# Performance work log

Measured on AMD Instinct MI355X. Metric: run time of the kernel, lower is better.

Reference implementation:

```python
import jax, jax.numpy as jnp
import numpy as np

SIGMA = 10.0   # collision energy scale (init sigma)
LCOL = 0.5     # collision length scale (init lcol)


def setup_inputs() -> dict:
    key = jax.random.key(0)
    B, D = 64, 2050  # 64 chains, N = 1 + (D-4)/2 = 1024 beads each
    # values must be in [-0.5, 0.5]: r2 = conf + 0.5 feeds arccos(1 - 2*r2)
    confdata = jax.random.uniform(key, (B, D), dtype=jnp.float32, minval=-0.5, maxval=0.5)
    return {"confdata": confdata}


def _energy(confdata):
    # --- get_poly, batched over all chains ---
    init_pos = confdata[:, 1:4]                      # [B, 3]
    c = confdata[:, 4:] + 0.5                        # [B, 2*(N-1)] in [0, 1]
    r1, r2 = c[:, ::2], c[:, 1::2]                   # [B, N-1]
    ph = r1 * (2.0 * jnp.pi)
    th = jnp.arccos(1.0 - 2.0 * r2)
    st = jnp.sin(th)
    steps = jnp.stack([st * jnp.cos(ph), st * jnp.sin(ph), jnp.cos(th)], axis=-1)  # [B, N-1, 3]
    pos = jnp.cumsum(jnp.concatenate([init_pos[:, None, :], steps], axis=1), axis=1)  # [B, N, 3]

    # --- collisions: sum over pairs with d > 0 of exp(-(d/lcol)^2) ---
    diff = pos[:, :, None, :] - pos[:, None, :, :]   # [B, N, N, 3]; exact zeros on diagonal
    d2 = jnp.sum(diff * diff, axis=-1)               # [B, N, N]
    e = jnp.where(d2 > 0, jnp.exp(-d2 / (LCOL * LCOL)), 0.0)
    return SIGMA * jnp.sum(e)


def reference(confdata):
    return _energy(confdata)
```

## Files before the change

kernel.cpp:

```cpp
#include <hip/hip_runtime.h>

#define NPOS 1024
#define NBATCH 64
#define DROW 2050
#define NPG 18
#define NBLK (NBATCH * NPG)

__global__ __launch_bounds__(256) void fused_kernel(const float* __restrict__ conf,
                                                    float* __restrict__ part) {
  __shared__ float4 P[NPOS];
  __shared__ float wsx[4], wsy[4], wsz[4];
  __shared__ float red[4];

  const int g = blockIdx.x % NPG;
  const int b = blockIdx.x / NPG;
  const int tid = threadIdx.x;
  const int lane = tid & 63, w = tid >> 6;
  const float* __restrict__ row = conf + b * DROW;
  const float ALPHA = 2.40224481f;

  float lx[4], ly[4], lz[4];
  float rx = 0.f, ry = 0.f, rz = 0.f;
#pragma unroll
  for (int k = 0; k < 4; ++k) {
    const int n = 4 * tid + k;
    if (n > 0) {
      const float2 rr = *reinterpret_cast<const float2*>(row + 2 + 2 * n);
      const float r1 = rr.x + 0.5f;
      const float r2 = rr.y + 0.5f;
      const float ct = 1.f - 2.f * r2;
      const float st = sqrtf(fmaxf(0.f, 1.f - ct * ct));
      const float sp = __builtin_amdgcn_sinf(r1);
      const float cp = __builtin_amdgcn_cosf(r1);
      rx += st * cp; ry += st * sp; rz += ct;
    }
    lx[k] = rx; ly[k] = ry; lz[k] = rz;
  }
  const float ttx = rx, tty = ry, ttz = rz;
  float sx = rx, sy = ry, sz = rz;
#pragma unroll
  for (int off = 1; off < 64; off <<= 1) {
    const float ax = __shfl_up(sx, off, 64);
    const float ay = __shfl_up(sy, off, 64);
    const float az = __shfl_up(sz, off, 64);
    if (lane >= off) { sx += ax; sy += ay; sz += az; }
  }
  if (lane == 63) { wsx[w] = sx; wsy[w] = sy; wsz[w] = sz; }
  __syncthreads();
  float cx = 0.f, cy = 0.f, cz = 0.f;
#pragma unroll
  for (int ww = 0; ww < 3; ++ww)
    if (ww < w) { cx += wsx[ww]; cy += wsy[ww]; cz += wsz[ww]; }

  const float ox = row[1] + cx + (sx - ttx);
  const float oy = row[2] + cy + (sy - tty);
  const float oz = row[3] + cz + (sz - ttz);
#pragma unroll
  for (int k = 0; k < 4; ++k) {
    const float X = ALPHA * (ox + lx[k]);
    const float Y = ALPHA * (oy + ly[k]);
    const float Z = ALPHA * (oz + lz[k]);
    float n2 = X * X; n2 = fmaf(Y, Y, n2); n2 = fmaf(Z, Z, n2);
    P[4 * tid + k] = make_float4(X, Y, Z, -n2);
  }
  __syncthreads();

  const int il = tid & 63;
  const int jq = w;
  float total = 0.f;
#pragma unroll
  for (int s = 0; s < 2; ++s) {
    const int p = 2 * g + s;
    int ci, cj;
    float wgt;
    if (p < 8) {
      ci = p; cj = p; wgt = 1.f;
    } else {
      int r = p - 8;
      ci = 0;
      while (r >= 7 - ci) { r -= 7 - ci; ++ci; }
      cj = ci + 1 + r; wgt = 2.f;
    }
    const float4 A = P[ci * 128 + il];
    const float4 B = P[ci * 128 + il + 64];
    const float dAx = 2.f * A.x, dAy = 2.f * A.y, dAz = 2.f * A.z;
    const float dBx = 2.f * B.x, dBy = 2.f * B.y, dBz = 2.f * B.z;
    const float4* __restrict__ Q = &P[cj * 128 + jq * 32];
    float a0 = 0.f, a1 = 0.f;
#pragma unroll 4
    for (int jj = 0; jj < 32; ++jj) {
      const float4 q = Q[jj];
      const float gA = fmaf(dAx, q.x, fmaf(dAy, q.y, fmaf(dAz, q.z, A.w + q.w)));
      const float gB = fmaf(dBx, q.x, fmaf(dBy, q.y, fmaf(dBz, q.z, B.w + q.w)));
      a0 += __builtin_amdgcn_exp2f(gA);
      a1 += __builtin_amdgcn_exp2f(gB);
    }
    total = fmaf(wgt, a0 + a1, total);
  }

#pragma unroll
  for (int off = 32; off; off >>= 1) total += __shfl_down(total, off, 64);
  if (lane == 0) red[w] = total;
  __syncthreads();
  if (tid == 0) part[blockIdx.x] = (red[0] + red[1]) + (red[2] + red[3]);
}

__global__ __launch_bounds__(256) void reduce_kernel(const float* __restrict__ part,
                                                     float* __restrict__ out) {
  float s = 0.f;
  for (int i = threadIdx.x; i < NBLK; i += 256) s += part[i];
#pragma unroll
  for (int off = 32; off; off >>= 1) s += __shfl_down(s, off, 64);
  __shared__ float red[4];
  const int lane = threadIdx.x & 63, w = threadIdx.x >> 6;
  if (lane == 0) red[w] = s;
  __syncthreads();
  if (threadIdx.x == 0) {
    out[0] = 10.0f * ((red[0] + red[1]) + (red[2] + red[3])) - 655360.0f;
  }
}

extern "C" void kernel_launch(void* const* d_in, const int* in_sizes, int n_in,
                              void* d_out, int out_size, void* d_ws, size_t ws_size,
                              hipStream_t stream) {
  const float* conf = (const float*)d_in[0];
  float* out = (float*)d_out;
  float* part = (float*)d_ws;
  hipLaunchKernelGGL(fused_kernel, dim3(NBLK), dim3(256), 0, stream, conf, part);
  hipLaunchKernelGGL(reduce_kernel, dim3(1), dim3(256), 0, stream, part, out);
}
```

Before: 19.13 us.

## Exploit pair symmetry in diagonal tiles to cut grid to 16 groups per chain

Diagonal 128x128 tiles are now computed as half-tiles with a circular offset scheme, so each unordered pair is evaluated once and self-pairs are skipped. The whole sum can then be doubled instead of subtracting the diagonal constant. This reduces the work per chain from 18 to 16 block-units and removes the redundant diagonal exp evaluations. The cost is modulo indexing and a branch inside the inner loop, plus possible LDS bank conflicts from the wrapped accesses.

```diff
diff --git a/kernel.cpp b/kernel.cpp
--- a/kernel.cpp
+++ b/kernel.cpp
@@ -3,8 +3,8 @@
 #define NPOS 1024
 #define NBATCH 64
 #define DROW 2050
-#define NPG 18
-#define NBLK (NBATCH * NPG)
+#define NGRP 16
+#define NBLK (NBATCH * NGRP)
 
 __global__ __launch_bounds__(256) void fused_kernel(const float* __restrict__ conf,
                                                     float* __restrict__ part) {
@@ -12,8 +12,8 @@
   __shared__ float wsx[4], wsy[4], wsz[4];
   __shared__ float red[4];
 
-  const int g = blockIdx.x % NPG;
-  const int b = blockIdx.x / NPG;
+  const int g = blockIdx.x % NGRP;
+  const int b = blockIdx.x / NGRP;
   const int tid = threadIdx.x;
   const int lane = tid & 63, w = tid >> 6;
   const float* __restrict__ row = conf + b * DROW;
@@ -66,36 +66,56 @@
   __syncthreads();
 
   const int il = tid & 63;
-  const int jq = w;
   float total = 0.f;
+
 #pragma unroll
   for (int s = 0; s < 2; ++s) {
-    const int p = 2 * g + s;
-    int ci, cj;
-    float wgt;
-    if (p < 8) {
-      ci = p; cj = p; wgt = 1.f;
+    const int u = 2 * g + s;
+    float a0 = 0.f, a1 = 0.f;
+    if (u < 4) {
+#pragma unroll
+      for (int h = 0; h < 2; ++h) {
+        const float4* __restrict__ C = &P[(2 * u + h) * 128];
+        const float4 A = C[il];
+        const float4 B = C[il + 64];
+        const float dAx = 2.f * A.x, dAy = 2.f * A.y, dAz = 2.f * A.z;
+        const float dBx = 2.f * B.x, dBy = 2.f * B.y, dBz = 2.f * B.z;
+        const int ob = w * 16;
+#pragma unroll 4
+        for (int oo = 1; oo <= 16; ++oo) {
+          const int o = ob + oo;
+          const float4 qa = C[(il + o) & 127];
+          const float4 qb = C[(il + 64 + o) & 127];
+          const float gA =
+              fmaf(dAx, qa.x, fmaf(dAy, qa.y, fmaf(dAz, qa.z, A.w + qa.w)));
+          const float gB =
+              fmaf(dBx, qb.x, fmaf(dBy, qb.y, fmaf(dBz, qb.z, B.w + qb.w)));
+          a0 += __builtin_amdgcn_exp2f(gA);
+          if (o != 64) a1 += __builtin_amdgcn_exp2f(gB);
+        }
+      }
     } else {
-      int r = p - 8;
-      ci = 0;
+      int r = u - 4;
+      int ci = 0;
       while (r >= 7 - ci) { r -= 7 - ci; ++ci; }
-      cj = ci + 1 + r; wgt = 2.f;
+      const int cj = ci + 1 + r;
+      const float4 A = P[ci * 128 + il];
+      const float4 B = P[ci * 128 + il + 64];
+      const float dAx = 2.f * A.x, dAy = 2.f * A.y, dAz = 2.f * A.z;
+      const float dBx = 2.f * B.x, dBy = 2.f * B.y, dBz = 2.f * B.z;
+      const float4* __restrict__ Q = &P[cj * 128 + w * 32];
+#pragma unroll 4
+      for (int jj = 0; jj < 32; ++jj) {
+        const float4 q = Q[jj];
+        const float gA =
+            fmaf(dAx, q.x, fmaf(dAy, q.y, fmaf(dAz, q.z, A.w + q.w)));
+        const float gB =
+            fmaf(dBx, q.x, fmaf(dBy, q.y, fmaf(dBz, q.z, B.w + q.w)));
+        a0 += __builtin_amdgcn_exp2f(gA);
+        a1 += __builtin_amdgcn_exp2f(gB);
+      }
     }
-    const float4 A = P[ci * 128 + il];
-    const float4 B = P[ci * 128 + il + 64];
-    const float dAx = 2.f * A.x, dAy = 2.f * A.y, dAz = 2.f * A.z;
-    const float dBx = 2.f * B.x, dBy = 2.f * B.y, dBz = 2.f * B.z;
-    const float4* __restrict__ Q = &P[cj * 128 + jq * 32];
-    float a0 = 0.f, a1 = 0.f;
-#pragma unroll 4
-    for (int jj = 0; jj < 32; ++jj) {
-      const float4 q = Q[jj];
-      const float gA = fmaf(dAx, q.x, fmaf(dAy, q.y, fmaf(dAz, q.z, A.w + q.w)));
-      const float gB = fmaf(dBx, q.x, fmaf(dBy, q.y, fmaf(dBz, q.z, B.w + q.w)));
-      a0 += __builtin_amdgcn_exp2f(gA);
-      a1 += __builtin_amdgcn_exp2f(gB);
-    }
-    total = fmaf(wgt, a0 + a1, total);
+    total += a0 + a1;
   }
 
 #pragma unroll
@@ -116,7 +136,7 @@
   if (lane == 0) red[w] = s;
   __syncthreads();
   if (threadIdx.x == 0) {
-    out[0] = 10.0f * ((red[0] + red[1]) + (red[2] + red[3])) - 655360.0f;
+    out[0] = 20.0f * ((red[0] + red[1]) + (red[2] + red[3]));
   }
 }
 
```

Result: slower. 19.67 us (+2.8%).
